# Optimization experiments

Hardware: AMD Instinct MI355X
Metric: run time of the kernel (lower is better)

The kernel has to match this reference:

```python
import jax, jax.numpy as jnp
import numpy as np

K = 20
EPS = 1e-5

def _lrelu(x):
    return jnp.where(x >= 0, x, 0.2 * x)

def _bn(x, g, b, m, v, axis=1):
    shp = [1] * x.ndim
    shp[axis] = -1
    scale = (g / jnp.sqrt(v + EPS)).reshape(shp)
    return (x - m.reshape(shp)) * scale + b.reshape(shp)

def _graph_feature(x, k):
    # x: [B, C, N] -> [B, 2C, N, k]  (kNN in feature space, concat(x_j - x_i, x_i))
    xx = jnp.sum(x * x, axis=1)                        # [B, N]
    inner = jnp.einsum('bcn,bcm->bnm', x, x)           # [B, N, N]
    neg_dist = 2.0 * inner - xx[:, :, None] - xx[:, None, :]
    _, idx = jax.lax.top_k(neg_dist, k)                # [B, N, k] nearest neighbors
    xt = jnp.transpose(x, (0, 2, 1))                   # [B, N, C]
    nb = jax.vmap(lambda f, i: f[i])(xt, idx)          # [B, N, k, C]
    center = jnp.broadcast_to(xt[:, :, None, :], nb.shape)
    feat = jnp.concatenate([nb - center, center], axis=-1)  # [B, N, k, 2C]
    return jnp.transpose(feat, (0, 3, 1, 2))

def _edge_block(x, w, g, b, m, v):
    # EdgeConv: graph feature -> 1x1 conv -> BN -> LeakyReLU -> max over k
    f = _graph_feature(x, K)                           # [B, 2C, N, k]
    y = jnp.einsum('oc,bcnk->bonk', w, f)
    y = _lrelu(_bn(y, g, b, m, v, 1))
    return jnp.max(y, axis=-1)                         # [B, O, N]


def setup_inputs() -> dict:
    key = jax.random.key(0)
    ks = iter(jax.random.split(key, 64))
    def randn(*s, scale=1.0):
        return jax.random.normal(next(ks), s, dtype=jnp.float32) * scale
    def unif(*s):
        return jax.random.uniform(next(ks), s, dtype=jnp.float32, minval=0.5, maxval=1.5)
    d = {}
    d['x'] = randn(16, 3, 1024)
    # conv / linear weights (fan-in scaled)
    for name, o, c in [('w1', 64, 6), ('w2', 64, 128), ('w3', 128, 128),
                       ('w4', 256, 256), ('w5', 1024, 512),
                       ('wl1', 512, 2048), ('wl2', 256, 512), ('wl3', 101, 256)]:
        d[name] = randn(o, c, scale=1.0 / np.sqrt(c))
    d['bl2'] = randn(256, scale=0.02)
    d['bl3'] = randn(101, scale=0.02)
    # BN params (eval-mode running stats)
    for i, c in [('1', 64), ('2', 64), ('3', 128), ('4', 256), ('5', 1024), ('6', 512), ('7', 256)]:
        d['g' + i] = 1.0 + randn(c, scale=0.1)
        d['b' + i] = randn(c, scale=0.1)
        d['m' + i] = randn(c, scale=0.1)
        d['v' + i] = unif(c)
    return d


def reference(x, w1, g1, b1, m1, v1, w2, g2, b2, m2, v2, w3, g3, b3, m3, v3,
              w4, g4, b4, m4, v4, w5, g5, b5, m5, v5,
              wl1, g6, b6, m6, v6, wl2, bl2, g7, b7, m7, v7, wl3, bl3):
    x1 = _edge_block(x,  w1, g1, b1, m1, v1)   # [B, 64, N]
    x2 = _edge_block(x1, w2, g2, b2, m2, v2)   # [B, 64, N]
    x3 = _edge_block(x2, w3, g3, b3, m3, v3)   # [B, 128, N]
    x4 = _edge_block(x3, w4, g4, b4, m4, v4)   # [B, 256, N]
    xc = jnp.concatenate([x1, x2, x3, x4], axis=1)           # [B, 512, N]
    y = _lrelu(_bn(jnp.einsum('oc,bcn->bon', w5, xc), g5, b5, m5, v5, 1))  # [B, 1024, N]
    p = jnp.concatenate([jnp.max(y, axis=-1), jnp.mean(y, axis=-1)], axis=1)  # [B, 2048]
    h = _lrelu(_bn(p @ wl1.T, g6, b6, m6, v6, 1))            # [B, 512]
    h = _lrelu(_bn(h @ wl2.T + bl2, g7, b7, m7, v7, 1))      # [B, 256]
    return h @ wl3.T + bl3                                   # [B, 101]
```

## Files before the change

kernel.cpp:

```cpp
#include <hip/hip_runtime.h>
#include <cstdint>
#include <cmath>

#define DI __device__ __forceinline__

constexpr int BB = 16;
constexpr int NN = 1024;
constexpr int KK = 20;
constexpr int NPT = BB*NN;
constexpr float EPSF = 1e-5f;
constexpr float NEGINF = -3.0e38f;

DI float lrelu(float x){ return x >= 0.f ? x : 0.2f * x; }
DI float dot4(const float4 a, const float4 b){ return a.x*b.x + a.y*b.y + a.z*b.z + a.w*b.w; }
DI unsigned short f2bf(float x){
    uint32_t u = __float_as_uint(x);
    uint32_t r = (u + 0x7fffu + ((u >> 16) & 1u)) >> 16;
    return (unsigned short)r;
}

DI float wave_max64(float v){
    v = fmaxf(v, __int_as_float(__builtin_amdgcn_mov_dpp(__float_as_int(v), 0x121, 0xF, 0xF, true)));
    v = fmaxf(v, __int_as_float(__builtin_amdgcn_mov_dpp(__float_as_int(v), 0x122, 0xF, 0xF, true)));
    v = fmaxf(v, __int_as_float(__builtin_amdgcn_mov_dpp(__float_as_int(v), 0x124, 0xF, 0xF, true)));
    v = fmaxf(v, __int_as_float(__builtin_amdgcn_mov_dpp(__float_as_int(v), 0x128, 0xF, 0xF, true)));
    v = fmaxf(v, __shfl_xor(v, 16));
    v = fmaxf(v, __shfl_xor(v, 32));
    return v;
}

typedef __attribute__((ext_vector_type(8))) short short8v;
typedef __attribute__((ext_vector_type(4))) float f32x4;

__global__ void k_transpose(const float* __restrict__ x, float* __restrict__ xt, float* __restrict__ xx)
{
    int i = blockIdx.x * 256 + threadIdx.x;
    if (i >= NPT) return;
    int b = i >> 10, n = i & 1023;
    float a = x[(b*3 + 0)*NN + n];
    float c = x[(b*3 + 1)*NN + n];
    float d = x[(b*3 + 2)*NN + n];
    xt[i*3 + 0] = a; xt[i*3 + 1] = c; xt[i*3 + 2] = d;
    xx[i] = a*a + c*c + d*d;
}

template<int C>
__global__ __launch_bounds__(1024, 4) void k_knn(const float* __restrict__ src, int stride,
                                                 const float* __restrict__ xx,
                                                 int* __restrict__ idxo)
{
    constexpr bool SMALL = (C == 3);
    constexpr int CG = SMALL ? 1 : (C / 4);
    constexpr int TS = SMALL ? 5 : C;
    constexpr int NBUF = SMALL ? 1 : 2;
    constexpr int LPT = SMALL ? 1 : (128*CG/1024);
    __shared__ float tile[NBUF][128 * TS];

    const int tid  = threadIdx.x;
    const int lane = tid & 63;
    const int wv   = __builtin_amdgcn_readfirstlane(tid >> 6);
    const int b  = blockIdx.x >> 4;
    const int q0 = (blockIdx.x & 15) << 6;
    const int qbase = b*NN + q0 + (wv << 2);

    const float* qp0 = src + (size_t)(qbase + 0)*stride;
    const float* qp1 = src + (size_t)(qbase + 1)*stride;
    const float* qp2 = src + (size_t)(qbase + 2)*stride;
    const float* qp3 = src + (size_t)(qbase + 3)*stride;

    float xxq[4];
    #pragma unroll
    for (int q = 0; q < 4; ++q) xxq[q] = xx[qbase + q];

    float val[4][16];

    if constexpr (SMALL){
        #pragma unroll
        for (int t = 0; t < 8; ++t){
            __syncthreads();
            for (int i = tid; i < 128*3; i += 1024){
                int row = i / 3, c = i % 3;
                tile[0][row*TS + c] = src[(size_t)(b*NN + t*128 + row)*stride + c];
            }
            __syncthreads();
            float c0a = tile[0][lane*TS+0], c0b = tile[0][lane*TS+1], c0c = tile[0][lane*TS+2];
            float c1a = tile[0][(64+lane)*TS+0], c1b = tile[0][(64+lane)*TS+1], c1c = tile[0][(64+lane)*TS+2];
            float q00 = qp0[0], q01 = qp0[1], q02 = qp0[2];
            float q10 = qp1[0], q11 = qp1[1], q12 = qp1[2];
            float q20 = qp2[0], q21 = qp2[1], q22 = qp2[2];
            float q30 = qp3[0], q31 = qp3[1], q32 = qp3[2];
            float xxm0 = xx[b*NN + t*128 + lane];
            float xxm1 = xx[b*NN + t*128 + 64 + lane];
            val[0][2*t]   = 2.f*(q00*c0a + q01*c0b + q02*c0c) - xxq[0] - xxm0;
            val[0][2*t+1] = 2.f*(q00*c1a + q01*c1b + q02*c1c) - xxq[0] - xxm1;
            val[1][2*t]   = 2.f*(q10*c0a + q11*c0b + q12*c0c) - xxq[1] - xxm0;
            val[1][2*t+1] = 2.f*(q10*c1a + q11*c1b + q12*c1c) - xxq[1] - xxm1;
            val[2][2*t]   = 2.f*(q20*c0a + q21*c0b + q22*c0c) - xxq[2] - xxm0;
            val[2][2*t+1] = 2.f*(q20*c1a + q21*c1b + q22*c1c) - xxq[2] - xxm1;
            val[3][2*t]   = 2.f*(q30*c0a + q31*c0b + q32*c0c) - xxq[3] - xxm0;
            val[3][2*t+1] = 2.f*(q30*c1a + q31*c1b + q32*c1c) - xxq[3] - xxm1;
        }
    } else {
        float4 nx[LPT];
        #pragma unroll
        for (int k = 0; k < LPT; ++k){
            int i = tid + k*1024;
            int row = i / CG, cg = i % CG;
            nx[k] = *(const float4*)(src + (size_t)(b*NN + row)*stride + cg*4);
        }
        #pragma unroll
        for (int k = 0; k < LPT; ++k){
            int i = tid + k*1024;
            int row = i / CG, cg = i % CG;
            int p = cg ^ (row & (CG - 1));
            *(float4*)(&tile[0][row*TS + p*4]) = nx[k];
        }

        for (int t = 0; t < 8; ++t){
            __syncthreads();
            if (t < 7){
                #pragma unroll
                for (int k = 0; k < LPT; ++k){
                    int i = tid + k*1024;
                    int row = i / CG, cg = i % CG;
                    nx[k] = *(const float4*)(src + (size_t)(b*NN + (t+1)*128 + row)*stride + cg*4);
                }
            }
            const float* tb = tile[t & 1];

            float acc[4][2];
            #pragma unroll
            for (int q = 0; q < 4; ++q){ acc[q][0] = 0.f; acc[q][1] = 0.f; }
            const int sw = lane & (CG - 1);
            #pragma unroll 2
            for (int cg0 = 0; cg0 < CG; ++cg0){
                float4 cf0 = *(const float4*)(tb + lane*TS      + ((cg0 ^ sw) << 2));
                float4 cf1 = *(const float4*)(tb + (64+lane)*TS + ((cg0 ^ sw) << 2));
                float4 qf0 = *(const float4*)(qp0 + (cg0 << 2));
                float4 qf1 = *(const float4*)(qp1 + (cg0 << 2));
                float4 qf2 = *(const float4*)(qp2 + (cg0 << 2));
                float4 qf3 = *(const float4*)(qp3 + (cg0 << 2));
                acc[0][0] += dot4(qf0, cf0); acc[0][1] += dot4(qf0, cf1);
                acc[1][0] += dot4(qf1, cf0); acc[1][1] += dot4(qf1, cf1);
                acc[2][0] += dot4(qf2, cf0); acc[2][1] += dot4(qf2, cf1);
                acc[3][0] += dot4(qf3, cf0); acc[3][1] += dot4(qf3, cf1);
            }
            float xxm0 = xx[b*NN + t*128 + lane];
            float xxm1 = xx[b*NN + t*128 + 64 + lane];
            #pragma unroll
            for (int q = 0; q < 4; ++q){
                val[q][2*t]   = 2.f*acc[q][0] - xxq[q] - xxm0;
                val[q][2*t+1] = 2.f*acc[q][1] - xxq[q] - xxm1;
            }

            if (t < 7){
                float* wb = &tile[(t+1) & 1][0];
                #pragma unroll
                for (int k = 0; k < LPT; ++k){
                    int i = tid + k*1024;
                    int row = i / CG, cg = i % CG;
                    int p = cg ^ (row & (CG - 1));
                    *(float4*)(&wb[row*TS + p*4]) = nx[k];
                }
            }
        }
    }

    #pragma unroll
    for (int q = 0; q < 4; ++q){
        const int orow = (qbase + q) * KK;

        float s[16];
        #pragma unroll
        for (int j = 0; j < 16; ++j) s[j] = val[q][j];
        #pragma unroll
        for (int k = 2; k <= 16; k <<= 1){
            #pragma unroll
            for (int jj = k >> 1; jj > 0; jj >>= 1){
                #pragma unroll
                for (int i = 0; i < 16; ++i){
                    int l = i ^ jj;
                    if (l > i){
                        float a = s[i], c = s[l];
                        float mx = fmaxf(a, c), mn = fminf(a, c);
                        bool up = ((i & k) == 0);
                        s[i] = up ? mx : mn;
                        s[l] = up ? mn : mx;
                    }
                }
            }
        }

        float T = NEGINF;
        for (int it = 0; it < 21; ++it){
            float m = wave_max64(s[0]);
            T = m;
            unsigned long long mk = __ballot(s[0] == m);
            int wl = __ffsll(mk) - 1;
            bool adv = (lane == wl);
            #pragma unroll
            for (int j = 0; j < 15; ++j) s[j] = adv ? s[j+1] : s[j];
            s[15] = adv ? NEGINF : s[15];
        }

        int cnt = 0;
        #pragma unroll
        for (int j = 0; j < 16; ++j) cnt += (val[q][j] > T) ? 1 : 0;
        int off = cnt;
        #pragma unroll
        for (int d = 1; d < 64; d <<= 1){
            int tt = __shfl_up(off, d);
            if (lane >= d) off += tt;
        }
        int total = __shfl(off, 63);
        int pos = orow + off - cnt;
        #pragma unroll
        for (int j = 0; j < 16; ++j){
            if (val[q][j] > T){ idxo[pos] = j*64 + lane; ++pos; }
        }
        if (total < KK){
            int rem = KK - total;
            int prior = 0;
            #pragma unroll
            for (int j = 0; j < 16; ++j){
                unsigned long long mk = __ballot(val[q][j] == T);
                int below = __popcll(mk & ((1ull << lane) - 1ull));
                if ((val[q][j] == T) && (prior + below < rem))
                    idxo[orow + total + prior + below] = j*64 + lane;
                prior += __popcll(mk);
            }
        }
    }
}

template<int K, int M2, int O, bool UB16>
__global__ __launch_bounds__(256) void k_uvgemm(const float* __restrict__ srcp,
    const float* __restrict__ w,
    const float* __restrict__ g, const float* __restrict__ bp,
    const float* __restrict__ mp, const float* __restrict__ vp,
    float* __restrict__ ub, float* __restrict__ xcv)
{
    constexpr int LD = 136;
    __shared__ float wl[16*LD];
    __shared__ float xl[16*LD];
    const int tid = threadIdx.x;
    const int nt = blockIdx.x & 127;
    const int mt = blockIdx.x >> 7;
    const int to = tid >> 4, tn = tid & 15;

    float acc[8][8];
    #pragma unroll
    for (int i = 0; i < 8; ++i)
        #pragma unroll
        for (int j = 0; j < 8; ++j) acc[i][j] = 0.f;

    for (int c0 = 0; c0 < K; c0 += 16){
        __syncthreads();
        #pragma unroll
        for (int p = 0; p < 2; ++p){
            int fi = tid + (p << 8);
            int row = fi >> 2, cq = (fi & 3) << 2;
            int gr = mt*128 + row;
            float4 wv;
            if (gr < O){
                wv = *(const float4*)(w + (size_t)gr*(2*K) + c0 + cq);
            } else {
                int o = gr - O;
                float4 a  = *(const float4*)(w + (size_t)o*(2*K) + c0 + cq);
                float4 bq = *(const float4*)(w + (size_t)o*(2*K) + K + c0 + cq);
                wv = make_float4(bq.x-a.x, bq.y-a.y, bq.z-a.z, bq.w-a.w);
            }
            wl[(cq+0)*LD + row] = wv.x;
            wl[(cq+1)*LD + row] = wv.y;
            wl[(cq+2)*LD + row] = wv.z;
            wl[(cq+3)*LD + row] = wv.w;
            float4 xv = *(const float4*)(srcp + (size_t)(nt*128 + row)*512 + c0 + cq);
            xl[(cq+0)*LD + row] = xv.x;
            xl[(cq+1)*LD + row] = xv.y;
            xl[(cq+2)*LD + row] = xv.z;
            xl[(cq+3)*LD + row] = xv.w;
        }
        __syncthreads();
        #pragma unroll
        for (int cc = 0; cc < 16; ++cc){
            float4 a0 = *(const float4*)(wl + cc*LD + to*8);
            float4 a1 = *(const float4*)(wl + cc*LD + to*8 + 4);
            float4 b0 = *(const float4*)(xl + cc*LD + tn*8);
            float4 b1 = *(const float4*)(xl + cc*LD + tn*8 + 4);
            float av[8] = {a0.x,a0.y,a0.z,a0.w,a1.x,a1.y,a1.z,a1.w};
            float bv[8] = {b0.x,b0.y,b0.z,b0.w,b1.x,b1.y,b1.z,b1.w};
            #pragma unroll
            for (int i = 0; i < 8; ++i)
                #pragma unroll
                for (int j = 0; j < 8; ++j) acc[i][j] += av[i]*bv[j];
        }
    }

    const int mbase = mt*128 + to*8;
    const bool isu = mbase < O;
    float mult[8], add[8];
    #pragma unroll
    for (int i = 0; i < 8; ++i){
        int m = mbase + i;
        if (isu){
            float s = g[m] / sqrtf(vp[m] + EPSF);
            mult[i] = (s >= 0.f) ? 1.f : -1.f;
            add[i]  = 0.f;
        } else {
            int o = m - O;
            float s = g[o] / sqrtf(vp[o] + EPSF);
            mult[i] = s;
            add[i]  = bp[o] - mp[o]*s;
        }
    }
    #pragma unroll
    for (int j = 0; j < 8; ++j){
        int pt = nt*128 + tn*8 + j;
        float4 v0, v1;
        v0.x = fmaf(mult[0], acc[0][j], add[0]);
        v0.y = fmaf(mult[1], acc[1][j], add[1]);
        v0.z = fmaf(mult[2], acc[2][j], add[2]);
        v0.w = fmaf(mult[3], acc[3][j], add[3]);
        v1.x = fmaf(mult[4], acc[4][j], add[4]);
        v1.y = fmaf(mult[5], acc[5][j], add[5]);
        v1.z = fmaf(mult[6], acc[6][j], add[6]);
        v1.w = fmaf(mult[7], acc[7][j], add[7]);
        if (isu){
            if constexpr (UB16){
                union { unsigned short u[8]; uint4 v; } o;
                o.u[0] = f2bf(v0.x); o.u[1] = f2bf(v0.y); o.u[2] = f2bf(v0.z); o.u[3] = f2bf(v0.w);
                o.u[4] = f2bf(v1.x); o.u[5] = f2bf(v1.y); o.u[6] = f2bf(v1.z); o.u[7] = f2bf(v1.w);
                *(uint4*)((unsigned short*)ub + (size_t)pt*O + mbase) = o.v;
            } else {
                float* d = ub + (size_t)pt*O + mbase;
                *(float4*)(d)     = v0;
                *(float4*)(d + 4) = v1;
            }
        } else {
            float* d = xcv + (size_t)pt*512 + (mbase - O);
            *(float4*)(d)     = v0;
            *(float4*)(d + 4) = v1;
        }
    }
}

__global__ __launch_bounds__(256) void k_uv3(const float* __restrict__ xt,
    const float* __restrict__ w,
    const float* __restrict__ g, const float* __restrict__ bp,
    const float* __restrict__ mp, const float* __restrict__ vp,
    float* __restrict__ ub, float* __restrict__ xcv)
{
    __shared__ float wpl[128*3];
    __shared__ float mult[128], add[128];
    const int tid = threadIdx.x;
    if (tid < 128){
        int m = tid;
        if (m < 64){
            float s = g[m] / sqrtf(vp[m] + EPSF);
            mult[m] = (s >= 0.f) ? 1.f : -1.f;
            add[m]  = 0.f;
        } else {
            int o = m - 64;
            float s = g[o] / sqrtf(vp[o] + EPSF);
            mult[m] = s;
            add[m]  = bp[o] - mp[o]*s;
        }
    }
    for (int i = tid; i < 128*3; i += 256){
        int m = i / 3, c = i % 3;
        wpl[i] = (m < 64) ? w[m*6 + c] : (w[(m-64)*6 + 3 + c] - w[(m-64)*6 + c]);
    }
    __syncthreads();

    const int ptl = tid >> 5, mg = tid & 31;
    const int m0 = mg * 4;
    const int pt = blockIdx.x*8 + ptl;
    float x0 = xt[pt*3+0], x1 = xt[pt*3+1], x2 = xt[pt*3+2];
    float4 v4;
    float tmp[4];
    #pragma unroll
    for (int r = 0; r < 4; ++r){
        int m = m0 + r;
        float a = wpl[m*3+0]*x0 + wpl[m*3+1]*x1 + wpl[m*3+2]*x2;
        tmp[r] = fmaf(mult[m], a, add[m]);
    }
    v4.x = tmp[0]; v4.y = tmp[1]; v4.z = tmp[2]; v4.w = tmp[3];
    if (m0 < 64) *(float4*)(ub + (size_t)pt*64 + m0) = v4;
    else         *(float4*)(xcv + (size_t)pt*512 + (m0 - 64)) = v4;
}

__global__ __launch_bounds__(256) void k_uvmfma(const float* __restrict__ xc,
    const float* __restrict__ w,
    const float* __restrict__ g, const float* __restrict__ bp,
    const float* __restrict__ mp, const float* __restrict__ vp,
    unsigned short* __restrict__ ub, float* __restrict__ vout)
{
    __shared__ __align__(16) short lA[128*32];
    __shared__ __align__(16) short lB[128*32];
    __shared__ float scl[128], adl[128];

    const int tid = threadIdx.x;
    const int lane = tid & 63, wave = tid >> 6;
    const int wm = wave >> 1, wn = wave & 1;
    const int mt = blockIdx.x >> 7;
    const int nt = blockIdx.x & 127;

    if (tid < 128){
        int m = mt*128 + tid;
        if (m < 256){
            float s = g[m] / sqrtf(vp[m] + EPSF);
            scl[tid] = (s >= 0.f) ? 1.f : -1.f;
            adl[tid] = 0.f;
        } else {
            int o = m - 256;
            float s = g[o] / sqrtf(vp[o] + EPSF);
            scl[tid] = s;
            adl[tid] = bp[o] - mp[o]*s;
        }
    }

    f32x4 acc[4][4];
    #pragma unroll
    for (int i = 0; i < 4; ++i)
        #pragma unroll
        for (int j = 0; j < 4; ++j) acc[i][j] = (f32x4){0.f,0.f,0.f,0.f};

    const bool isu = (mt < 2);

    for (int ks = 0; ks < 4; ++ks){
        __syncthreads();
        #pragma unroll
        for (int p = 0; p < 2; ++p){
            int off = p*256 + tid;
            int row = off >> 2;
            int slot = off & 3;
            int ssl = slot ^ (row & 3);
            float va[8];
            if (isu){
                int m = mt*128 + row;
                const float* sp = w + (size_t)m*256 + ks*32 + slot*8;
                float4 a0 = *(const float4*)(sp);
                float4 a1 = *(const float4*)(sp + 4);
                va[0]=a0.x; va[1]=a0.y; va[2]=a0.z; va[3]=a0.w;
                va[4]=a1.x; va[5]=a1.y; va[6]=a1.z; va[7]=a1.w;
            } else {
                int o = (mt-2)*128 + row;
                const float* sp = w + (size_t)o*256 + ks*32 + slot*8;
                float4 a0 = *(const float4*)(sp);
                float4 a1 = *(const float4*)(sp + 4);
                float4 b0 = *(const float4*)(sp + 128);
                float4 b1 = *(const float4*)(sp + 132);
                va[0]=b0.x-a0.x; va[1]=b0.y-a0.y; va[2]=b0.z-a0.z; va[3]=b0.w-a0.w;
                va[4]=b1.x-a1.x; va[5]=b1.y-a1.y; va[6]=b1.z-a1.z; va[7]=b1.w-a1.w;
            }
            union { unsigned short u[8]; uint4 v; } oa;
            #pragma unroll
            for (int e = 0; e < 8; ++e) oa.u[e] = f2bf(va[e]);
            *(uint4*)(lA + row*32 + ssl*8) = oa.v;
            const float* spb = xc + (size_t)(nt*128 + row)*512 + 128 + ks*32 + slot*8;
            float4 x0 = *(const float4*)(spb);
            float4 x1 = *(const float4*)(spb + 4);
            union { unsigned short u[8]; uint4 v; } ob;
            ob.u[0]=f2bf(x0.x); ob.u[1]=f2bf(x0.y); ob.u[2]=f2bf(x0.z); ob.u[3]=f2bf(x0.w);
            ob.u[4]=f2bf(x1.x); ob.u[5]=f2bf(x1.y); ob.u[6]=f2bf(x1.z); ob.u[7]=f2bf(x1.w);
            *(uint4*)(lB + row*32 + ssl*8) = ob.v;
        }
        __syncthreads();

        short8v afr[4], bfr[4];
        #pragma unroll
        for (int i = 0; i < 4; ++i){
            int row = wm*64 + i*16 + (lane & 15);
            int sl  = (lane >> 4) ^ (row & 3);
            afr[i] = *(const short8v*)(lA + row*32 + sl*8);
        }
        #pragma unroll
        for (int j = 0; j < 4; ++j){
            int row = wn*64 + j*16 + (lane & 15);
            int sl  = (lane >> 4) ^ (row & 3);
            bfr[j] = *(const short8v*)(lB + row*32 + sl*8);
        }
        #pragma unroll
        for (int i = 0; i < 4; ++i)
            #pragma unroll
            for (int j = 0; j < 4; ++j)
                acc[i][j] = __builtin_amdgcn_mfma_f32_16x16x32_bf16(afr[i], bfr[j], acc[i][j], 0, 0, 0);
    }

    #pragma unroll
    for (int i = 0; i < 4; ++i){
        #pragma unroll
        for (int j = 0; j < 4; ++j){
            int m_loc = wm*64 + i*16 + (lane >> 4)*4;
            int pt    = nt*128 + wn*64 + j*16 + (lane & 15);
            if (isu){
                union { unsigned short u[4]; uint2 v; } o;
                #pragma unroll
                for (int r = 0; r < 4; ++r)
                    o.u[r] = f2bf(scl[m_loc + r] * acc[i][j][r]);
                *(uint2*)(ub + (size_t)pt*256 + mt*128 + m_loc) = o.v;
            } else {
                float4 y;
                y.x = fmaf(scl[m_loc+0], acc[i][j][0], adl[m_loc+0]);
                y.y = fmaf(scl[m_loc+1], acc[i][j][1], adl[m_loc+1]);
                y.z = fmaf(scl[m_loc+2], acc[i][j][2], adl[m_loc+2]);
                y.w = fmaf(scl[m_loc+3], acc[i][j][3], adl[m_loc+3]);
                *(float4*)(vout + (size_t)pt*512 + (mt-2)*128 + m_loc) = y;
            }
        }
    }
}

template<int O, bool UB16, bool NORM>
__global__ __launch_bounds__(256) void k_edgemax(const float* __restrict__ ub,
    const int* __restrict__ idxg,
    const float* __restrict__ g, const float* __restrict__ vp,
    float* __restrict__ xcv, float* __restrict__ xxout)
{
    constexpr int TPP = O / 4;
    constexpr int PPB = 256 / TPP;
    const int tid = threadIdx.x;
    const int pt  = blockIdx.x*PPB + tid / TPP;
    const int oq  = (tid % TPP) * 4;
    const int bb  = pt & ~(NN-1);

    int nb[KK];
    #pragma unroll
    for (int k = 0; k < KK; ++k) nb[k] = idxg[pt*KK + k];

    float4 mx;
    if constexpr (UB16){
        const unsigned short* ubh = (const unsigned short*)ub;
        uint2 r0 = *(const uint2*)(ubh + (size_t)(bb + nb[0])*O + oq);
        mx.x = __uint_as_float(r0.x << 16);
        mx.y = __uint_as_float(r0.x & 0xffff0000u);
        mx.z = __uint_as_float(r0.y << 16);
        mx.w = __uint_as_float(r0.y & 0xffff0000u);
        #pragma unroll
        for (int k = 1; k < KK; ++k){
            uint2 r = *(const uint2*)(ubh + (size_t)(bb + nb[k])*O + oq);
            mx.x = fmaxf(mx.x, __uint_as_float(r.x << 16));
            mx.y = fmaxf(mx.y, __uint_as_float(r.x & 0xffff0000u));
            mx.z = fmaxf(mx.z, __uint_as_float(r.y << 16));
            mx.w = fmaxf(mx.w, __uint_as_float(r.y & 0xffff0000u));
        }
    } else {
        mx = *(const float4*)(ub + (size_t)(bb + nb[0])*O + oq);
        #pragma unroll
        for (int k = 1; k < KK; ++k){
            float4 u = *(const float4*)(ub + (size_t)(bb + nb[k])*O + oq);
            mx.x = fmaxf(mx.x, u.x); mx.y = fmaxf(mx.y, u.y);
            mx.z = fmaxf(mx.z, u.z); mx.w = fmaxf(mx.w, u.w);
        }
    }
    float4 gv = *(const float4*)(g + oq);
    float4 vv = *(const float4*)(vp + oq);
    float4 as;
    as.x = fabsf(gv.x / sqrtf(vv.x + EPSF));
    as.y = fabsf(gv.y / sqrtf(vv.y + EPSF));
    as.z = fabsf(gv.z / sqrtf(vv.z + EPSF));
    as.w = fabsf(gv.w / sqrtf(vv.w + EPSF));
    float* d = xcv + (size_t)pt*512 + oq;
    float4 vr = *(const float4*)(d);
    float4 y;
    y.x = lrelu(fmaf(as.x, mx.x, vr.x));
    y.y = lrelu(fmaf(as.y, mx.y, vr.y));
    y.z = lrelu(fmaf(as.z, mx.z, vr.z));
    y.w = lrelu(fmaf(as.w, mx.w, vr.w));
    *(float4*)(d) = y;

    if constexpr (NORM){
        float part = dot4(y, y);
        #pragma unroll
        for (int dd = 1; dd < TPP; dd <<= 1) part += __shfl_xor(part, dd);
        if ((tid & (TPP - 1)) == 0) xxout[pt] = part;
    }
}

__global__ __launch_bounds__(256) void k_conv5mfma(const float* __restrict__ xc,
    const float* __restrict__ w5,
    const float* __restrict__ g, const float* __restrict__ bp,
    const float* __restrict__ mp, const float* __restrict__ vp,
    float* __restrict__ pmax, float* __restrict__ psum)
{
    __shared__ __align__(16) short lA[128*32];
    __shared__ __align__(16) short lB[128*32];
    __shared__ float scl[128], adl[128];
    __shared__ float red[2][128][2];

    const int tid = threadIdx.x;
    const int lane = tid & 63, wave = tid >> 6;
    const int wm = wave >> 1, wn = wave & 1;
    const int b  = blockIdx.x >> 6;
    const int mt = (blockIdx.x >> 3) & 7;
    const int nt = blockIdx.x & 7;

    if (tid < 128){
        int o = mt*128 + tid;
        float s = g[o] / sqrtf(vp[o] + EPSF);
        scl[tid] = s;
        adl[tid] = bp[o] - mp[o]*s;
    }

    f32x4 acc[4][4];
    #pragma unroll
    for (int i = 0; i < 4; ++i)
        #pragma unroll
        for (int j = 0; j < 4; ++j) acc[i][j] = (f32x4){0.f,0.f,0.f,0.f};

    const float* gA = w5 + (size_t)(mt*128)*512;
    const float* gB = xc + (size_t)(b*1024 + nt*128)*512;

    for (int ks = 0; ks < 16; ++ks){
        __syncthreads();
        #pragma unroll
        for (int p = 0; p < 2; ++p){
            int off = p*256 + tid;
            int row = off >> 2;
            int slot = off & 3;
            int ssl = slot ^ (row & 3);
            const float* spa = gA + (size_t)row*512 + ks*32 + slot*8;
            float4 a0 = *(const float4*)(spa);
            float4 a1 = *(const float4*)(spa + 4);
            union { unsigned short u[8]; uint4 v; } oa;
            oa.u[0]=f2bf(a0.x); oa.u[1]=f2bf(a0.y); oa.u[2]=f2bf(a0.z); oa.u[3]=f2bf(a0.w);
            oa.u[4]=f2bf(a1.x); oa.u[5]=f2bf(a1.y); oa.u[6]=f2bf(a1.z); oa.u[7]=f2bf(a1.w);
            *(uint4*)(lA + row*32 + ssl*8) = oa.v;
            const float* spb = gB + (size_t)row*512 + ks*32 + slot*8;
            float4 x0 = *(const float4*)(spb);
            float4 x1 = *(const float4*)(spb + 4);
            union { unsigned short u[8]; uint4 v; } ob;
            ob.u[0]=f2bf(x0.x); ob.u[1]=f2bf(x0.y); ob.u[2]=f2bf(x0.z); ob.u[3]=f2bf(x0.w);
            ob.u[4]=f2bf(x1.x); ob.u[5]=f2bf(x1.y); ob.u[6]=f2bf(x1.z); ob.u[7]=f2bf(x1.w);
            *(uint4*)(lB + row*32 + ssl*8) = ob.v;
        }
        __syncthreads();

        short8v afr[4], bfr[4];
        #pragma unroll
        for (int i = 0; i < 4; ++i){
            int row = wm*64 + i*16 + (lane & 15);
            int sl  = (lane >> 4) ^ (row & 3);
            afr[i] = *(const short8v*)(lA + row*32 + sl*8);
        }
        #pragma unroll
        for (int j = 0; j < 4; ++j){
            int row = wn*64 + j*16 + (lane & 15);
            int sl  = (lane >> 4) ^ (row & 3);
            bfr[j] = *(const short8v*)(lB + row*32 + sl*8);
        }
        #pragma unroll
        for (int i = 0; i < 4; ++i)
            #pragma unroll
            for (int j = 0; j < 4; ++j)
                acc[i][j] = __builtin_amdgcn_mfma_f32_16x16x32_bf16(afr[i], bfr[j], acc[i][j], 0, 0, 0);
    }

    float emx[4][4], esm[4][4];
    #pragma unroll
    for (int i = 0; i < 4; ++i){
        #pragma unroll
        for (int r = 0; r < 4; ++r){
            int m_loc = wm*64 + i*16 + (lane >> 4)*4 + r;
            float s = scl[m_loc], t = adl[m_loc];
            float mx = NEGINF, sm = 0.f;
            #pragma unroll
            for (int j = 0; j < 4; ++j){
                float y = lrelu(fmaf(acc[i][j][r], s, t));
                mx = fmaxf(mx, y); sm += y;
            }
            #pragma unroll
            for (int d = 1; d < 16; d <<= 1){
                mx = fmaxf(mx, __shfl_xor(mx, d));
                sm += __shfl_xor(sm, d);
            }
            emx[i][r] = mx; esm[i][r] = sm;
        }
    }
    if ((lane & 15) == 0){
        #pragma unroll
        for (int i = 0; i < 4; ++i)
            #pragma unroll
            for (int r = 0; r < 4; ++r){
                int m_loc = wm*64 + i*16 + (lane >> 4)*4 + r;
                red[wn][m_loc][0] = emx[i][r];
                red[wn][m_loc][1] = esm[i][r];
            }
    }
    __syncthreads();
    if (tid < 128){
        float mx = fmaxf(red[0][tid][0], red[1][tid][0]);
        float sm = red[0][tid][1] + red[1][tid][1];
        int o = mt*128 + tid;
        pmax[(size_t)(b*NN + o)*8 + nt] = mx;
        psum[(size_t)(b*NN + o)*8 + nt] = sm;
    }
}

__global__ void k_poolfin(const float* __restrict__ pmax, const float* __restrict__ psum,
                          float* __restrict__ p)
{
    int i = blockIdx.x*256 + threadIdx.x;
    if (i >= NPT) return;
    int b = i >> 10, o = i & 1023;
    float mx = NEGINF, sm = 0.f;
    #pragma unroll
    for (int t = 0; t < 8; ++t){ mx = fmaxf(mx, pmax[(size_t)i*8 + t]); sm += psum[(size_t)i*8 + t]; }
    p[b*2048 + o]        = mx;
    p[b*2048 + 1024 + o] = sm * (1.f/1024.f);
}

template<int IN, int O, bool HASBN, bool HASBIAS>
__global__ void k_fc(const float* __restrict__ in, const float* __restrict__ W,
                     const float* __restrict__ bias,
                     const float* __restrict__ g, const float* __restrict__ bp,
                     const float* __restrict__ mp, const float* __restrict__ vp,
                     float* __restrict__ out)
{
    int i = blockIdx.x*256 + threadIdx.x;
    if (i >= BB*O) return;
    int b = i / O, o = i % O;
    const float* wr = W  + (size_t)o*IN;
    const float* ir = in + (size_t)b*IN;
    float s = 0.f;
    #pragma unroll 4
    for (int c = 0; c < IN; c += 4){
        float4 a = *(const float4*)(wr + c);
        float4 x = *(const float4*)(ir + c);
        s += dot4(a, x);
    }
    if (HASBIAS) s += bias[o];
    if (HASBN){
        float sc = g[o] / sqrtf(vp[o] + EPSF);
        s = (s - mp[o])*sc + bp[o];
        s = lrelu(s);
    }
    out[(size_t)b*O + o] = s;
}

extern "C" void kernel_launch(void* const* d_in, const int* in_sizes, int n_in,
                              void* d_out, int out_size, void* d_ws, size_t ws_size,
                              hipStream_t stream)
{
    (void)in_sizes; (void)n_in; (void)out_size; (void)ws_size;
    const float* x   = (const float*)d_in[0];
    const float* w1  = (const float*)d_in[1];
    const float* w2  = (const float*)d_in[2];
    const float* w3  = (const float*)d_in[3];
    const float* w4  = (const float*)d_in[4];
    const float* w5  = (const float*)d_in[5];
    const float* wl1 = (const float*)d_in[6];
    const float* wl2 = (const float*)d_in[7];
    const float* wl3 = (const float*)d_in[8];
    const float* bl2 = (const float*)d_in[9];
    const float* bl3 = (const float*)d_in[10];
    const float* g1 = (const float*)d_in[11]; const float* b1 = (const float*)d_in[12];
    const float* m1 = (const float*)d_in[13]; const float* v1 = (const float*)d_in[14];
    const float* g2 = (const float*)d_in[15]; const float* b2 = (const float*)d_in[16];
    const float* m2 = (const float*)d_in[17]; const float* v2 = (const float*)d_in[18];
    const float* g3 = (const float*)d_in[19]; const float* b3 = (const float*)d_in[20];
    const float* m3 = (const float*)d_in[21]; const float* v3 = (const float*)d_in[22];
    const float* g4 = (const float*)d_in[23]; const float* b4 = (const float*)d_in[24];
    const float* m4 = (const float*)d_in[25]; const float* v4 = (const float*)d_in[26];
    const float* g5 = (const float*)d_in[27]; const float* b5 = (const float*)d_in[28];
    const float* m5 = (const float*)d_in[29]; const float* v5 = (const float*)d_in[30];
    const float* g6 = (const float*)d_in[31]; const float* b6 = (const float*)d_in[32];
    const float* m6 = (const float*)d_in[33]; const float* v6 = (const float*)d_in[34];
    const float* g7 = (const float*)d_in[35]; const float* b7 = (const float*)d_in[36];
    const float* m7 = (const float*)d_in[37]; const float* v7 = (const float*)d_in[38];

    float* wsf  = (float*)d_ws;
    float* xt0  = wsf;
    float* xc   = xt0 + 49152;
    float* xx   = xc + 8388608;
    int*   idx  = (int*)(xx + 16384);
    float* pmax = (float*)(idx + 327680);
    float* psum = pmax + 131072;
    float* p    = psum + 131072;
    float* h1   = p + 32768;
    float* h2   = h1 + 8192;
    float* ub   = h2 + 4096;

    k_transpose<<<64, 256, 0, stream>>>(x, xt0, xx);

    k_knn<3><<<256, 1024, 0, stream>>>(xt0, 3, xx, idx);
    k_uv3<<<2048, 256, 0, stream>>>(xt0, w1, g1, b1, m1, v1, ub, xc);
    k_edgemax<64, false, true><<<1024, 256, 0, stream>>>(ub, idx, g1, v1, xc, xx);

    k_knn<64><<<256, 1024, 0, stream>>>(xc, 512, xx, idx);
    k_uvgemm<64, 128, 64, false><<<128, 256, 0, stream>>>(xc, w2, g2, b2, m2, v2, ub, xc + 64);
    k_edgemax<64, false, true><<<1024, 256, 0, stream>>>(ub, idx, g2, v2, xc + 64, xx);

    k_knn<64><<<256, 1024, 0, stream>>>(xc + 64, 512, xx, idx);
    k_uvgemm<64, 256, 128, false><<<256, 256, 0, stream>>>(xc + 64, w3, g3, b3, m3, v3, ub, xc + 128);
    k_edgemax<128, false, true><<<2048, 256, 0, stream>>>(ub, idx, g3, v3, xc + 128, xx);

    k_knn<128><<<256, 1024, 0, stream>>>(xc + 128, 512, xx, idx);
    k_uvmfma<<<512, 256, 0, stream>>>(xc, w4, g4, b4, m4, v4, (unsigned short*)ub, xc + 256);
    k_edgemax<256, true, false><<<4096, 256, 0, stream>>>(ub, idx, g4, v4, xc + 256, nullptr);

    k_conv5mfma<<<1024, 256, 0, stream>>>(xc, w5, g5, b5, m5, v5, pmax, psum);
    k_poolfin<<<64, 256, 0, stream>>>(pmax, psum, p);

    k_fc<2048, 512, true,  false><<<32, 256, 0, stream>>>(p,  wl1, nullptr, g6, b6, m6, v6, h1);
    k_fc<512,  256, true,  true ><<<16, 256, 0, stream>>>(h1, wl2, bl2,     g7, b7, m7, v7, h2);
    k_fc<256,  101, false, true ><<<7,  256, 0, stream>>>(h2, wl3, bl3, nullptr, nullptr, nullptr, nullptr, (float*)d_out);
}
```

Measured before the change: 522.0 us.

## Split kNN distance work across wave pairs with 8 queries each and LDS exchange

For the non-small kNN path, each pair of waves now handles 8 query points, and each wave computes distances for only half of the candidate tiles. This doubles query reuse per loaded candidate float4 and halves per-wave distance work. The partial distance rows are then swapped through shared memory so each wave holds 4 full query rows for the top-k selection. The cost is a larger shared buffer (128KB of floats, likely limiting occupancy), more registers for 8 query accumulators, and idle halves of the t loop per wave.

```diff
diff --git a/kernel.cpp b/kernel.cpp
--- a/kernel.cpp
+++ b/kernel.cpp
@@ -52,39 +52,36 @@
     constexpr bool SMALL = (C == 3);
     constexpr int CG = SMALL ? 1 : (C / 4);
     constexpr int TS = SMALL ? 5 : C;
-    constexpr int NBUF = SMALL ? 1 : 2;
     constexpr int LPT = SMALL ? 1 : (128*CG/1024);
-    __shared__ float tile[NBUF][128 * TS];
+    __shared__ float smem[SMALL ? 1024 : 32768];
 
     const int tid  = threadIdx.x;
     const int lane = tid & 63;
-    const int wv   = __builtin_amdgcn_readfirstlane(tid >> 6);
+    const int w    = __builtin_amdgcn_readfirstlane(tid >> 6);
     const int b  = blockIdx.x >> 4;
     const int q0 = (blockIdx.x & 15) << 6;
-    const int qbase = b*NN + q0 + (wv << 2);
-
-    const float* qp0 = src + (size_t)(qbase + 0)*stride;
-    const float* qp1 = src + (size_t)(qbase + 1)*stride;
-    const float* qp2 = src + (size_t)(qbase + 2)*stride;
-    const float* qp3 = src + (size_t)(qbase + 3)*stride;
-
-    float xxq[4];
-    #pragma unroll
-    for (int q = 0; q < 4; ++q) xxq[q] = xx[qbase + q];
-
-    float val[4][16];
 
     if constexpr (SMALL){
+        const int qbase = b*NN + q0 + (w << 2);
+        const float* qp0 = src + (size_t)(qbase + 0)*3;
+        const float* qp1 = src + (size_t)(qbase + 1)*3;
+        const float* qp2 = src + (size_t)(qbase + 2)*3;
+        const float* qp3 = src + (size_t)(qbase + 3)*3;
+        float xxq[4];
+        #pragma unroll
+        for (int q = 0; q < 4; ++q) xxq[q] = xx[qbase + q];
+
+        float val[4][16];
         #pragma unroll
         for (int t = 0; t < 8; ++t){
             __syncthreads();
             for (int i = tid; i < 128*3; i += 1024){
                 int row = i / 3, c = i % 3;
-                tile[0][row*TS + c] = src[(size_t)(b*NN + t*128 + row)*stride + c];
+                smem[row*TS + c] = src[(size_t)(b*NN + t*128 + row)*3 + c];
             }
             __syncthreads();
-            float c0a = tile[0][lane*TS+0], c0b = tile[0][lane*TS+1], c0c = tile[0][lane*TS+2];
-            float c1a = tile[0][(64+lane)*TS+0], c1b = tile[0][(64+lane)*TS+1], c1c = tile[0][(64+lane)*TS+2];
+            float c0a = smem[lane*TS+0], c0b = smem[lane*TS+1], c0c = smem[lane*TS+2];
+            float c1a = smem[(64+lane)*TS+0], c1b = smem[(64+lane)*TS+1], c1c = smem[(64+lane)*TS+2];
             float q00 = qp0[0], q01 = qp0[1], q02 = qp0[2];
             float q10 = qp1[0], q11 = qp1[1], q12 = qp1[2];
             float q20 = qp2[0], q21 = qp2[1], q22 = qp2[2];
@@ -100,79 +97,174 @@
             val[3][2*t]   = 2.f*(q30*c0a + q31*c0b + q32*c0c) - xxq[3] - xxm0;
             val[3][2*t+1] = 2.f*(q30*c1a + q31*c1b + q32*c1c) - xxq[3] - xxm1;
         }
+
+        #pragma unroll
+        for (int q = 0; q < 4; ++q){
+            const int orow = (qbase + q) * KK;
+            float s[16];
+            #pragma unroll
+            for (int j = 0; j < 16; ++j) s[j] = val[q][j];
+            #pragma unroll
+            for (int k = 2; k <= 16; k <<= 1){
+                #pragma unroll
+                for (int jj = k >> 1; jj > 0; jj >>= 1){
+                    #pragma unroll
+                    for (int i = 0; i < 16; ++i){
+                        int l = i ^ jj;
+                        if (l > i){
+                            float a = s[i], c = s[l];
+                            float mx = fmaxf(a, c), mn = fminf(a, c);
+                            bool up = ((i & k) == 0);
+                            s[i] = up ? mx : mn;
+                            s[l] = up ? mn : mx;
+                        }
+                    }
+                }
+            }
+            float T = NEGINF;
+            for (int it = 0; it < 21; ++it){
+                float m = wave_max64(s[0]);
+                T = m;
+                unsigned long long mk = __ballot(s[0] == m);
+                bool adv = (lane == __ffsll(mk) - 1);
+                #pragma unroll
+                for (int j = 0; j < 15; ++j) s[j] = adv ? s[j+1] : s[j];
+                s[15] = adv ? NEGINF : s[15];
+            }
+            int cnt = 0;
+            #pragma unroll
+            for (int j = 0; j < 16; ++j) cnt += (val[q][j] > T) ? 1 : 0;
+            int off = cnt;
+            #pragma unroll
+            for (int d = 1; d < 64; d <<= 1){
+                int tt = __shfl_up(off, d);
+                if (lane >= d) off += tt;
+            }
+            int total = __shfl(off, 63);
+            int pos = orow + off - cnt;
+            #pragma unroll
+            for (int j = 0; j < 16; ++j){
+                if (val[q][j] > T){ idxo[pos] = j*64 + lane; ++pos; }
+            }
+            if (total < KK){
+                int rem = KK - total;
+                int prior = 0;
+                #pragma unroll
+                for (int j = 0; j < 16; ++j){
+                    unsigned long long mk = __ballot(val[q][j] == T);
+                    int below = __popcll(mk & ((1ull << lane) - 1ull));
+                    if ((val[q][j] == T) && (prior + below < rem))
+                        idxo[orow + total + prior + below] = j*64 + lane;
+                    prior += __popcll(mk);
+                }
+            }
+        }
+        return;
     } else {
-        float4 nx[LPT];
-        #pragma unroll
-        for (int k = 0; k < LPT; ++k){
-            int i = tid + k*1024;
-            int row = i / CG, cg = i % CG;
-            nx[k] = *(const float4*)(src + (size_t)(b*NN + row)*stride + cg*4);
-        }
-        #pragma unroll
-        for (int k = 0; k < LPT; ++k){
-            int i = tid + k*1024;
-            int row = i / CG, cg = i % CG;
-            int p = cg ^ (row & (CG - 1));
-            *(float4*)(&tile[0][row*TS + p*4]) = nx[k];
-        }
-
-        for (int t = 0; t < 8; ++t){
-            __syncthreads();
-            if (t < 7){
-                #pragma unroll
-                for (int k = 0; k < LPT; ++k){
-                    int i = tid + k*1024;
-                    int row = i / CG, cg = i % CG;
-                    nx[k] = *(const float4*)(src + (size_t)(b*NN + (t+1)*128 + row)*stride + cg*4);
-                }
-            }
-            const float* tb = tile[t & 1];
-
-            float acc[4][2];
-            #pragma unroll
-            for (int q = 0; q < 4; ++q){ acc[q][0] = 0.f; acc[q][1] = 0.f; }
+
+    const int g = w >> 1, h = w & 1;
+    const int qbaseg = b*NN + q0 + g*8;
+    const float* qp[8];
+    #pragma unroll
+    for (int q = 0; q < 8; ++q) qp[q] = src + (size_t)(qbaseg + q)*stride;
+    float xxq[8];
+    #pragma unroll
+    for (int q = 0; q < 8; ++q) xxq[q] = xx[qbaseg + q];
+
+    float val[8][8];
+
+    float4 nx[LPT];
+    #pragma unroll
+    for (int k = 0; k < LPT; ++k){
+        int i = tid + k*1024;
+        int row = i / CG, cg = i % CG;
+        nx[k] = *(const float4*)(src + (size_t)(b*NN + row)*stride + cg*4);
+    }
+    #pragma unroll
+    for (int k = 0; k < LPT; ++k){
+        int i = tid + k*1024;
+        int row = i / CG, cg = i % CG;
+        int p = cg ^ (row & (CG - 1));
+        *(float4*)(&smem[row*TS + p*4]) = nx[k];
+    }
+
+    for (int t = 0; t < 8; ++t){
+        __syncthreads();
+        if (t < 7){
+            #pragma unroll
+            for (int k = 0; k < LPT; ++k){
+                int i = tid + k*1024;
+                int row = i / CG, cg = i % CG;
+                nx[k] = *(const float4*)(src + (size_t)(b*NN + (t+1)*128 + row)*stride + cg*4);
+            }
+        }
+        if ((t >> 2) == h){
+            const int tl = t & 3;
+            const float* tb = smem + (t & 1)*128*TS;
+            float acc[8][2];
+            #pragma unroll
+            for (int q = 0; q < 8; ++q){ acc[q][0] = 0.f; acc[q][1] = 0.f; }
             const int sw = lane & (CG - 1);
-            #pragma unroll 2
             for (int cg0 = 0; cg0 < CG; ++cg0){
                 float4 cf0 = *(const float4*)(tb + lane*TS      + ((cg0 ^ sw) << 2));
                 float4 cf1 = *(const float4*)(tb + (64+lane)*TS + ((cg0 ^ sw) << 2));
-                float4 qf0 = *(const float4*)(qp0 + (cg0 << 2));
-                float4 qf1 = *(const float4*)(qp1 + (cg0 << 2));
-                float4 qf2 = *(const float4*)(qp2 + (cg0 << 2));
-                float4 qf3 = *(const float4*)(qp3 + (cg0 << 2));
-                acc[0][0] += dot4(qf0, cf0); acc[0][1] += dot4(qf0, cf1);
-                acc[1][0] += dot4(qf1, cf0); acc[1][1] += dot4(qf1, cf1);
-                acc[2][0] += dot4(qf2, cf0); acc[2][1] += dot4(qf2, cf1);
-                acc[3][0] += dot4(qf3, cf0); acc[3][1] += dot4(qf3, cf1);
+                #pragma unroll
+                for (int q = 0; q < 8; ++q){
+                    float4 qf = *(const float4*)(qp[q] + (cg0 << 2));
+                    acc[q][0] += dot4(qf, cf0);
+                    acc[q][1] += dot4(qf, cf1);
+                }
             }
             float xxm0 = xx[b*NN + t*128 + lane];
             float xxm1 = xx[b*NN + t*128 + 64 + lane];
             #pragma unroll
-            for (int q = 0; q < 4; ++q){
-                val[q][2*t]   = 2.f*acc[q][0] - xxq[q] - xxm0;
-                val[q][2*t+1] = 2.f*acc[q][1] - xxq[q] - xxm1;
-            }
-
-            if (t < 7){
-                float* wb = &tile[(t+1) & 1][0];
-                #pragma unroll
-                for (int k = 0; k < LPT; ++k){
-                    int i = tid + k*1024;
-                    int row = i / CG, cg = i % CG;
-                    int p = cg ^ (row & (CG - 1));
-                    *(float4*)(&wb[row*TS + p*4]) = nx[k];
-                }
-            }
-        }
-    }
-
-    #pragma unroll
-    for (int q = 0; q < 4; ++q){
-        const int orow = (qbase + q) * KK;
+            for (int q = 0; q < 8; ++q){
+                val[q][2*tl]   = 2.f*acc[q][0] - xxq[q] - xxm0;
+                val[q][2*tl+1] = 2.f*acc[q][1] - xxq[q] - xxm1;
+            }
+        }
+        if (t < 7){
+            float* wb = smem + ((t+1) & 1)*128*TS;
+            #pragma unroll
+            for (int k = 0; k < LPT; ++k){
+                int i = tid + k*1024;
+                int row = i / CG, cg = i % CG;
+                int p = cg ^ (row & (CG - 1));
+                *(float4*)(&wb[row*TS + p*4]) = nx[k];
+            }
+        }
+    }
+
+    const int keep0 = h*4, give0 = 4 - h*4;
+    __syncthreads();
+    #pragma unroll
+    for (int qq = 0; qq < 4; ++qq)
+        #pragma unroll
+        for (int j = 0; j < 8; ++j)
+            smem[((w*4 + qq)*8 + j)*64 + lane] = val[give0 + qq][j];
+    __syncthreads();
+
+    #pragma unroll
+    for (int qq = 0; qq < 4; ++qq){
+        const int orow = (qbaseg + keep0 + qq) * KK;
+        float v16[16];
+        if (h == 0){
+            #pragma unroll
+            for (int j = 0; j < 8; ++j){
+                v16[j]     = val[qq][j];
+                v16[8 + j] = smem[(((w^1)*4 + qq)*8 + j)*64 + lane];
+            }
+        } else {
+            #pragma unroll
+            for (int j = 0; j < 8; ++j){
+                v16[j]     = smem[(((w^1)*4 + qq)*8 + j)*64 + lane];
+                v16[8 + j] = val[4 + qq][j];
+            }
+        }
 
         float s[16];
         #pragma unroll
-        for (int j = 0; j < 16; ++j) s[j] = val[q][j];
+        for (int j = 0; j < 16; ++j) s[j] = v16[j];
         #pragma unroll
         for (int k = 2; k <= 16; k <<= 1){
             #pragma unroll
@@ -196,8 +288,7 @@
             float m = wave_max64(s[0]);
             T = m;
             unsigned long long mk = __ballot(s[0] == m);
-            int wl = __ffsll(mk) - 1;
-            bool adv = (lane == wl);
+            bool adv = (lane == __ffsll(mk) - 1);
             #pragma unroll
             for (int j = 0; j < 15; ++j) s[j] = adv ? s[j+1] : s[j];
             s[15] = adv ? NEGINF : s[15];
@@ -205,7 +296,7 @@
 
         int cnt = 0;
         #pragma unroll
-        for (int j = 0; j < 16; ++j) cnt += (val[q][j] > T) ? 1 : 0;
+        for (int j = 0; j < 16; ++j) cnt += (v16[j] > T) ? 1 : 0;
         int off = cnt;
         #pragma unroll
         for (int d = 1; d < 64; d <<= 1){
@@ -216,20 +307,21 @@
         int pos = orow + off - cnt;
         #pragma unroll
         for (int j = 0; j < 16; ++j){
-            if (val[q][j] > T){ idxo[pos] = j*64 + lane; ++pos; }
+            if (v16[j] > T){ idxo[pos] = j*64 + lane; ++pos; }
         }
         if (total < KK){
             int rem = KK - total;
             int prior = 0;
             #pragma unroll
             for (int j = 0; j < 16; ++j){
-                unsigned long long mk = __ballot(val[q][j] == T);
+                unsigned long long mk = __ballot(v16[j] == T);
                 int below = __popcll(mk & ((1ull << lane) - 1ull));
-                if ((val[q][j] == T) && (prior + below < rem))
+                if ((v16[j] == T) && (prior + below < rem))
                     idxo[orow + total + prior + below] = j*64 + lane;
                 prior += __popcll(mk);
             }
         }
+    }
     }
 }
 
```

New measurement: 713.6 us. +36.7%, slower.
